# Optimization experiments

Hardware: AMD Instinct MI355X
Metric: run time of the kernel (lower is better)

Reference implementation:

```python
import jax, jax.numpy as jnp
import numpy as np
import math

B, N, DIM = 4, 2048, 512
HEADS, DIM_HEAD = 8, 64
INNER = HEADS * DIM_HEAD  # 512


def setup_inputs() -> dict:
    key = jax.random.key(0)
    ks = jax.random.split(key, 4)
    x = jax.random.normal(ks[0], (B, N, DIM), dtype=jnp.float32)
    # nn.Linear(dim, inner*4, bias=False): store as [dim, 4*inner] for x @ W
    w_qkvg = jax.random.normal(ks[1], (DIM, 4 * INNER), dtype=jnp.float32) * (1.0 / math.sqrt(DIM))
    sigma = jnp.full((1, HEADS, 1, 1), 1.92, dtype=jnp.float32)
    w_out = jax.random.normal(ks[2], (2 * INNER, DIM), dtype=jnp.float32) * (1.0 / math.sqrt(2 * INNER))
    b_out = jax.random.normal(ks[3], (DIM,), dtype=jnp.float32) * 0.01
    return {"x": x, "w_qkvg": w_qkvg, "sigma": sigma, "w_out": w_out, "b_out": b_out}


def reference(x, w_qkvg, sigma, w_out, b_out):
    b, n, d = x.shape
    h, dh = HEADS, DIM_HEAD
    scale = dh ** (-0.5)

    qkvg = x @ w_qkvg  # [b, n, 4*inner]
    q, k, vg, vsigma = jnp.split(qkvg, 4, axis=-1)

    def to_heads(t):  # [b, n, h*dh] -> [b, h, n, dh]
        return t.reshape(b, n, h, dh).transpose(0, 2, 1, 3)

    q, k, vg, vsigma = map(to_heads, (q, k, vg, vsigma))

    # --- softmax branch ---
    dots = jnp.einsum('bhid,bhjd->bhij', q, k) * scale  # [b, h, n, n]
    corr_g = jax.nn.softmax(dots, axis=-1)
    out_g = jnp.matmul(corr_g, vg)  # [b, h, n, dh]

    # --- Gaussian positional-mask branch ---
    pos = jnp.arange(1, n + 1, dtype=x.dtype)
    diffs = jnp.abs(pos[:, None] - pos[None, :])  # [n, n]
    inv_norm = 1.0 / (jnp.sqrt(jnp.asarray(2.0 * math.pi, x.dtype)) * sigma)  # [1, h, 1, 1]
    gm = inv_norm * jnp.exp(-(diffs ** 2)[None, None] / (2.0 * sigma ** 2))  # [1, h, n, n]
    corr_sigma = gm / gm.sum(-1, keepdims=True)
    out_s = jnp.matmul(corr_sigma, vsigma)  # broadcasts over batch -> [b, h, n, dh]

    out = jnp.concatenate([out_g, out_s], axis=-1)  # [b, h, n, 2*dh]
    out = out.transpose(0, 2, 1, 3).reshape(b, n, 2 * h * dh)
    return out @ w_out + b_out
```

## Files before the change

kernel.cpp:

```cpp
#include <hip/hip_runtime.h>

typedef _Float16 f16;
typedef __attribute__((ext_vector_type(8))) _Float16 f16x8;
typedef __attribute__((ext_vector_type(4))) _Float16 f16x4;
typedef __attribute__((ext_vector_type(4))) float f32x4;

#define B_ 4
#define N_ 2048
#define DIM_ 512
#define H_ 8
#define DH_ 64

__device__ __forceinline__ void gload16(const void* g, void* l) {
    __builtin_amdgcn_global_load_lds((const __attribute__((address_space(1))) void*)g,
                                     (__attribute__((address_space(3))) void*)l, 16, 0, 0);
}


__global__ __launch_bounds__(256) void cvt_f16_k8(const float* __restrict__ in,
                                                  f16* __restrict__ out, int n8) {
    int i = blockIdx.x * 256 + threadIdx.x;
    if (i < n8) {
        const float4 a = ((const float4*)in)[i * 2];
        const float4 b = ((const float4*)in)[i * 2 + 1];
        f16x8 o = {(f16)a.x, (f16)a.y, (f16)a.z, (f16)a.w,
                   (f16)b.x, (f16)b.y, (f16)b.z, (f16)b.w};
        ((f16x8*)out)[i] = o;
    }
}

__global__ __launch_bounds__(256) void transpose_cvt_k(const float* __restrict__ in,
                                                       f16* __restrict__ out, int K, int N) {
    __shared__ f16 tile[64][72];
    const int nbk = K >> 6;
    const int bk = blockIdx.x % nbk, bn = blockIdx.x / nbk;
    const int k0 = bk << 6, n0 = bn << 6;
    const int t = threadIdx.x;
    const int r = t >> 2, q = (t & 3) << 4;
#pragma unroll
    for (int u = 0; u < 4; u++) {
        const float4 v = *(const float4*)&in[(size_t)(k0 + r) * N + n0 + q + u * 4];
        tile[q + u * 4 + 0][r] = (f16)v.x;
        tile[q + u * 4 + 1][r] = (f16)v.y;
        tile[q + u * 4 + 2][r] = (f16)v.z;
        tile[q + u * 4 + 3][r] = (f16)v.w;
    }
    __syncthreads();
#pragma unroll
    for (int u = 0; u < 2; u++) {
        f16x8 o = *(const f16x8*)&tile[r][q + u * 8];
        *(f16x8*)&out[(size_t)(n0 + r) * K + k0 + q + u * 8] = o;
    }
}

__global__ __launch_bounds__(512, 2) void gemm0_8ph(
    const f16* __restrict__ A, const f16* __restrict__ BT,
    f16* __restrict__ qb, f16* __restrict__ kb, f16* __restrict__ vbT,
    f16* __restrict__ vs16)
{
    __shared__ char lds[131072];
    const int tid = threadIdx.x;
    const int bid = blockIdx.x;
    const int xcd = bid & 7, w = bid >> 3;
    const int m0 = ((xcd << 2) + (w >> 3)) << 8;
    const int n0 = (w & 7) << 8;
    const int wave = tid >> 6, lane = tid & 63;
    const int wr = wave >> 2, wc = wave & 3;
    const int lr = lane & 15, lg = lane >> 4;

    f32x4 acc[8][4];
    const f32x4 zero = {0.f, 0.f, 0.f, 0.f};
#pragma unroll
    for (int i = 0; i < 8; i++)
#pragma unroll
        for (int j = 0; j < 4; j++) acc[i][j] = zero;

    const f16* gA[2][2]; const f16* gB[2][2];
#pragma unroll
    for (int u = 0; u < 2; u++) {
        int c = tid + u * 512;
        int row = c >> 3;
        int e0 = (((c & 7) ^ (row & 7)) << 3);
#pragma unroll
        for (int h = 0; h < 2; h++) {
            gA[h][u] = A + (size_t)(m0 + h * 128 + row) * 512 + e0;
            gB[h][u] = BT + (size_t)(n0 + h * 128 + row) * 512 + e0;
        }
    }
    const int ldst = wave * 1024;

#pragma unroll
    for (int h = 0; h < 2; h++)
#pragma unroll
        for (int u = 0; u < 2; u++)
            gload16(gA[h][u], lds + h * 16384 + ldst + u * 8192);
#pragma unroll
    for (int h = 0; h < 2; h++)
#pragma unroll
        for (int u = 0; u < 2; u++)
            gload16(gB[h][u], lds + 65536 + h * 16384 + ldst + u * 8192);

    const int swz = (lr & 7) << 4;
    for (int T = 0; T < 8; T++) {
        const int d = T & 1, d2 = (T + 1) & 1;
        const size_t Tn64 = (size_t)(T + 1) * 64;
        const char* Ab = lds + (d * 2 + wr) * 16384;
        const char* Bb = lds + 65536 + (d * 2 + (wc >> 1)) * 16384;
#pragma unroll
        for (int p = 0; p < 4; p++) {
            const int kh = p >> 1, qr = p & 1;
            if (p < 2) {
#pragma unroll
                for (int u = 0; u < 2; u++)
                    gload16(gA[p][u] + Tn64, lds + (d2 * 2 + p) * 16384 + ldst + u * 8192);
            } else {
#pragma unroll
                for (int u = 0; u < 2; u++)
                    gload16(gB[p - 2][u] + Tn64, lds + 65536 + (d2 * 2 + (p - 2)) * 16384 + ldst + u * 8192);
            }
            if (p == 0) {
                asm volatile("s_waitcnt vmcnt(2)" ::: "memory");
            }
            __builtin_amdgcn_s_barrier();

            f16x8 af[4], bf[4];
            const int ko = (kh * 64 + lg * 16) ^ swz;
#pragma unroll
            for (int i = 0; i < 4; i++)
                af[i] = *(const f16x8*)(Ab + (qr * 64 + i * 16 + lr) * 128 + ko);
#pragma unroll
            for (int j = 0; j < 4; j++)
                bf[j] = *(const f16x8*)(Bb + ((wc & 1) * 64 + j * 16 + lr) * 128 + ko);
            asm volatile("s_waitcnt lgkmcnt(0)" ::: "memory");
            __builtin_amdgcn_sched_barrier(0);
            __builtin_amdgcn_s_setprio(1);
#pragma unroll
            for (int i = 0; i < 4; i++)
#pragma unroll
                for (int j = 0; j < 4; j++)
                    acc[qr * 4 + i][j] = __builtin_amdgcn_mfma_f32_16x16x32_f16(af[i], bf[j], acc[qr * 4 + i][j], 0, 0, 0);
            __builtin_amdgcn_s_setprio(0);
            __builtin_amdgcn_s_barrier();
        }
    }

#pragma unroll
    for (int fr = 0; fr < 8; fr++) {
#pragma unroll
        for (int j = 0; j < 4; j++) {
            int col = n0 + wc * 64 + j * 16 + lr;
            int row0 = m0 + wr * 128 + fr * 16 + lg * 4;
            int sec = col >> 9, cc = col & 511;
            int h = cc >> 6, dd = cc & 63;
            int b = row0 >> 11, ns = row0 & 2047;
            if (sec == 2) {
                f16x4 o;
#pragma unroll
                for (int r = 0; r < 4; r++) o[r] = (f16)acc[fr][j][r];
                *(f16x4*)&vbT[((size_t)(b * H_ + h) * DH_ + dd) * N_ + ns] = o;
            } else if (sec == 0) {
#pragma unroll
                for (int r = 0; r < 4; r++)
                    qb[((size_t)(b * H_ + h) * N_ + ns + r) * DH_ + dd] = (f16)(acc[fr][j][r] * 0.1803368801f);
            } else if (sec == 1) {
#pragma unroll
                for (int r = 0; r < 4; r++)
                    kb[((size_t)(b * H_ + h) * N_ + ns + r) * DH_ + dd] = (f16)acc[fr][j][r];
            } else {
#pragma unroll
                for (int r = 0; r < 4; r++)
                    vs16[((size_t)(b * H_ + h) * N_ + ns + r) * DH_ + dd] = (f16)acc[fr][j][r];
            }
        }
    }
}

__global__ __launch_bounds__(256) void gemm_small(
    const f16* __restrict__ A, const f16* __restrict__ BT, int K, int N,
    const float* __restrict__ bias, float* __restrict__ outp)
{
    __shared__ char sAb[8192];
    __shared__ char sBb[8192];
    const int tid = threadIdx.x;
    const int bid = blockIdx.x;
    const int xcd = bid & 7, w = bid >> 3;
    const int m0 = ((xcd << 4) + (w >> 3)) << 6;
    const int n0 = (w & 7) << 6;
    const int wave = tid >> 6, lane = tid & 63;
    const int wr = wave >> 1, wc = wave & 1;
    const int lr = lane & 15, lg = lane >> 4;

    f32x4 acc[2][2];
    const f32x4 zero = {0.f, 0.f, 0.f, 0.f};
#pragma unroll
    for (int i = 0; i < 2; i++)
#pragma unroll
        for (int j = 0; j < 2; j++) acc[i][j] = zero;

    const f16* srcA[2]; const f16* srcB[2];
    char* ldsA[2]; char* ldsB[2];
#pragma unroll
    for (int u = 0; u < 2; u++) {
        int row = wave * 8 + u * 32 + (lane >> 3);
        int e0 = ((lane & 7) ^ (row & 7)) << 3;
        srcA[u] = A + (size_t)(m0 + row) * K + e0;
        srcB[u] = BT + (size_t)(n0 + row) * K + e0;
        ldsA[u] = sAb + wave * 1024 + u * 4096;
        ldsB[u] = sBb + wave * 1024 + u * 4096;
    }

    const int swz = (lr & 7) << 4;
    for (int kt = 0; kt < K; kt += 64) {
#pragma unroll
        for (int u = 0; u < 2; u++) {
            gload16(srcA[u], ldsA[u]);
            gload16(srcB[u], ldsB[u]);
            srcA[u] += 64; srcB[u] += 64;
        }
        __syncthreads();
#pragma unroll
        for (int half = 0; half < 2; half++) {
            f16x8 af[2], bf[2];
#pragma unroll
            for (int i = 0; i < 2; i++) {
                int R = wr * 32 + i * 16 + lr;
                af[i] = *(const f16x8*)(sAb + R * 128 + (((half << 6) | (lg << 4)) ^ swz));
            }
#pragma unroll
            for (int j = 0; j < 2; j++) {
                int R = wc * 32 + j * 16 + lr;
                bf[j] = *(const f16x8*)(sBb + R * 128 + (((half << 6) | (lg << 4)) ^ swz));
            }
#pragma unroll
            for (int i = 0; i < 2; i++)
#pragma unroll
                for (int j = 0; j < 2; j++)
                    acc[i][j] = __builtin_amdgcn_mfma_f32_16x16x32_f16(af[i], bf[j], acc[i][j], 0, 0, 0);
        }
        __syncthreads();
    }

#pragma unroll
    for (int i = 0; i < 2; i++)
#pragma unroll
        for (int j = 0; j < 2; j++) {
            int col = n0 + wc * 32 + j * 16 + lr;
            int row0 = m0 + wr * 32 + i * 16 + lg * 4;
#pragma unroll
            for (int r = 0; r < 4; r++)
                outp[(size_t)(row0 + r) * N + col] = acc[i][j][r] + bias[col];
        }
}

__global__ __launch_bounds__(256) void attn_k(
    const f16* __restrict__ qb, const f16* __restrict__ kb, const f16* __restrict__ vbT,
    f16* __restrict__ cat, f16* __restrict__ oaccB, float* __restrict__ lacc)
{
    __shared__ char sKbf[2 * 8192];
    __shared__ char sVbf[2 * 8192];
    const int tid = threadIdx.x;
    const int bid0 = blockIdx.x;
    const int obid = (bid0 & 7) * 128 + (bid0 >> 3);
    const int bh = obid >> 5, qblk = (obid >> 1) & 15, half = obid & 1;
    const int b = bh >> 3, h = bh & 7;
    const int hn = half << 4;
    const int wave = tid >> 6, lane = tid & 63;
    const int lr = lane & 15, lg = lane >> 4;

    const size_t base = (size_t)bh * N_ * DH_;
    const int qrow_a = qblk * 128 + wave * 32 + lr;
    const int qrow_b = qrow_a + 16;
    const f16x8 qfa0 = *(const f16x8*)&qb[base + (size_t)qrow_a * DH_ + lg * 8];
    const f16x8 qfa1 = *(const f16x8*)&qb[base + (size_t)qrow_a * DH_ + 32 + lg * 8];
    const f16x8 qfb0 = *(const f16x8*)&qb[base + (size_t)qrow_b * DH_ + lg * 8];
    const f16x8 qfb1 = *(const f16x8*)&qb[base + (size_t)qrow_b * DH_ + 32 + lg * 8];

    const f16* kq[2]; const f16* vq[2];
#pragma unroll
    for (int u = 0; u < 2; u++) {
        int row = wave * 8 + u * 32 + (lane >> 3);
        int e0 = ((lane & 7) ^ (row & 7)) << 3;
        kq[u] = kb + base + (size_t)row * 64 + e0;
        vq[u] = vbT + base + (size_t)row * 2048 + e0;
    }
    char* const ldsKw = sKbf + wave * 1024;
    char* const ldsVw = sVbf + wave * 1024;

    f32x4 Ota[4], Otb[4], lacc_a, lacc_b;
    const f32x4 zero = {0.f, 0.f, 0.f, 0.f};
#pragma unroll
    for (int dt = 0; dt < 4; dt++) { Ota[dt] = zero; Otb[dt] = zero; }
    lacc_a = zero; lacc_b = zero;
    const f16x8 ones8 = {(f16)1.f, (f16)1.f, (f16)1.f, (f16)1.f,
                         (f16)1.f, (f16)1.f, (f16)1.f, (f16)1.f};

    const int swz = (lr & 7) << 4;

#pragma unroll
    for (int u = 0; u < 2; u++) gload16(kq[u] + (size_t)hn * 4096, ldsKw + u * 4096);
#pragma unroll
    for (int u = 0; u < 2; u++) gload16(vq[u] + hn * 64, ldsVw + u * 4096);
    asm volatile("s_waitcnt vmcnt(0)" ::: "memory");
    __builtin_amdgcn_s_barrier();

    for (int t = 0; t < 16; t++) {
        {
            const int tn = hn + ((t + 1) & 15);
            char* vdst = ldsVw + ((t + 1) & 1) * 8192;
            char* kdst = ldsKw + ((t + 1) & 1) * 8192;
#pragma unroll
            for (int u = 0; u < 2; u++) gload16(vq[u] + tn * 64, vdst + u * 4096);
#pragma unroll
            for (int u = 0; u < 2; u++) gload16(kq[u] + (size_t)tn * 4096, kdst + u * 4096);
        }

        const char* Kb = sKbf + (t & 1) * 8192;
        const char* Vb = sVbf + (t & 1) * 8192;

        f32x4 sta[4], stb[4];
        __builtin_amdgcn_s_setprio(1);
#pragma unroll
        for (int ct = 0; ct < 4; ct++) {
            int row = ct * 16 + lr;
            f16x8 kf0 = *(const f16x8*)(Kb + (((row << 7) | (lg << 4)) ^ swz));
            f16x8 kf1 = *(const f16x8*)(Kb + (((row << 7) | 64 | (lg << 4)) ^ swz));
            f32x4 sa = __builtin_amdgcn_mfma_f32_16x16x32_f16(kf0, qfa0, zero, 0, 0, 0);
            sta[ct]  = __builtin_amdgcn_mfma_f32_16x16x32_f16(kf1, qfa1, sa, 0, 0, 0);
            f32x4 sb = __builtin_amdgcn_mfma_f32_16x16x32_f16(kf0, qfb0, zero, 0, 0, 0);
            stb[ct]  = __builtin_amdgcn_mfma_f32_16x16x32_f16(kf1, qfb1, sb, 0, 0, 0);
        }
        __builtin_amdgcn_s_setprio(0);

        f16x4 ppa[4], ppb[4];
#pragma unroll
        for (int ct = 0; ct < 4; ct++)
#pragma unroll
            for (int r = 0; r < 4; r++) {
                ppa[ct][r] = (f16)__builtin_amdgcn_exp2f(sta[ct][r]);
                ppb[ct][r] = (f16)__builtin_amdgcn_exp2f(stb[ct][r]);
            }

        __builtin_amdgcn_s_setprio(1);
#pragma unroll
        for (int c = 0; c < 2; c++) {
            f16x8 bfa = __builtin_shufflevector(ppa[2 * c], ppa[2 * c + 1], 0, 1, 2, 3, 4, 5, 6, 7);
            f16x8 bfb = __builtin_shufflevector(ppb[2 * c], ppb[2 * c + 1], 0, 1, 2, 3, 4, 5, 6, 7);
            lacc_a = __builtin_amdgcn_mfma_f32_16x16x32_f16(ones8, bfa, lacc_a, 0, 0, 0);
            lacc_b = __builtin_amdgcn_mfma_f32_16x16x32_f16(ones8, bfb, lacc_b, 0, 0, 0);
#pragma unroll
            for (int dt = 0; dt < 4; dt++) {
                int row = dt * 16 + lr;
                f16x4 vlo = *(const f16x4*)(Vb + (((row << 7) | (c << 6) | (lg << 3)) ^ swz));
                f16x4 vhi = *(const f16x4*)(Vb + (((row << 7) | (c << 6) | 32 | (lg << 3)) ^ swz));
                f16x8 vf = __builtin_shufflevector(vlo, vhi, 0, 1, 2, 3, 4, 5, 6, 7);
                Ota[dt] = __builtin_amdgcn_mfma_f32_16x16x32_f16(vf, bfa, Ota[dt], 0, 0, 0);
                Otb[dt] = __builtin_amdgcn_mfma_f32_16x16x32_f16(vf, bfb, Otb[dt], 0, 0, 0);
            }
        }
        __builtin_amdgcn_s_setprio(0);

        asm volatile("s_waitcnt vmcnt(0)" ::: "memory");
        __builtin_amdgcn_s_barrier();
    }

#pragma unroll
    for (int dt = 0; dt < 4; dt++) {
        f16x4 oa, ob;
#pragma unroll
        for (int r = 0; r < 4; r++) {
            oa[r] = (f16)Ota[dt][r];
            ob[r] = (f16)Otb[dt][r];
        }
        if (half == 0) {
            *(f16x4*)&cat[((size_t)(b * N_ + qrow_a)) * 1024 + h * 128 + dt * 16 + lg * 4] = oa;
            *(f16x4*)&cat[((size_t)(b * N_ + qrow_b)) * 1024 + h * 128 + dt * 16 + lg * 4] = ob;
        } else {
            *(f16x4*)&oaccB[((size_t)(bh * N_ + qrow_a)) * 64 + dt * 16 + lg * 4] = oa;
            *(f16x4*)&oaccB[((size_t)(bh * N_ + qrow_b)) * 64 + dt * 16 + lg * 4] = ob;
        }
    }
    if (lg == 0) {
        lacc[half * (32 * N_) + bh * N_ + qrow_a] = lacc_a[0];
        lacc[half * (32 * N_) + bh * N_ + qrow_b] = lacc_b[0];
    }
}

__global__ __launch_bounds__(256) void combine_k(
    f16* __restrict__ cat, const f16* __restrict__ oaccB, const float* __restrict__ lacc)
{
    int gi = blockIdx.x * 256 + threadIdx.x;
    int row = gi >> 3, c8 = gi & 7;
    int bh = row >> 11, q = row & 2047;
    int b = bh >> 3, h = bh & 7;
    float inv = 1.0f / (lacc[row] + lacc[32 * N_ + row]);
    f16* cp = &cat[((size_t)(b * N_ + q)) * 1024 + h * 128 + c8 * 8];
    f16x8 a = *(const f16x8*)cp;
    f16x8 o2 = *(const f16x8*)&oaccB[(size_t)row * 64 + c8 * 8];
    f16x8 o;
#pragma unroll
    for (int i = 0; i < 8; i++) o[i] = (f16)(((float)a[i] + (float)o2[i]) * inv);
    *(f16x8*)cp = o;
}

__global__ __launch_bounds__(256) void gauss_k(
    const f16* __restrict__ vs16, const float* __restrict__ sigma, f16* __restrict__ cat)
{
    const int tid = threadIdx.x;
    const int bh = blockIdx.y, b = bh >> 3, h = bh & 7;
    const int i0 = blockIdx.x * 64;
    const int wv = tid >> 6, d = tid & 63;
    const float sig = sigma[h];
    const float c = 0.72134752f / (sig * sig);

    float wt[17];
#pragma unroll
    for (int o = 0; o <= 16; o++) wt[o] = __builtin_amdgcn_exp2f(-(float)(o * o) * c);
    float wfull = wt[0];
#pragma unroll
    for (int o = 1; o <= 16; o++) wfull += 2.f * wt[o];
    const float inv_wfull = 1.0f / wfull;

    const size_t base = (size_t)bh * N_ * DH_;
    const int r0 = i0 + wv * 16 - 16;
    float v[48];
#pragma unroll
    for (int k = 0; k < 48; k++) {
        int r = r0 + k; r = r < 0 ? 0 : (r > N_ - 1 ? N_ - 1 : r);
        v[k] = (float)vs16[base + (size_t)r * DH_ + d];
    }

#pragma unroll
    for (int it = 0; it < 16; it++) {
        int i = i0 + wv * 16 + it;
        float acc = 0.f;
        if (i >= 16 && i <= N_ - 17) {
#pragma unroll
            for (int o = -16; o <= 16; o++)
                acc += wt[o < 0 ? -o : o] * v[16 + it + o];
            acc *= inv_wfull;
        } else {
            float ws = 0.f;
#pragma unroll
            for (int o = -16; o <= 16; o++) {
                int j = i + o;
                if (j >= 0 && j <= N_ - 1) {
                    float w = wt[o < 0 ? -o : o];
                    ws += w;
                    acc += w * v[16 + it + o];
                }
            }
            acc /= ws;
        }
        cat[((size_t)(b * N_ + i)) * 1024 + h * 128 + 64 + d] = (f16)acc;
    }
}


extern "C" void kernel_launch(void* const* d_in, const int* in_sizes, int n_in,
                              void* d_out, int out_size, void* d_ws, size_t ws_size,
                              hipStream_t stream) {
    const float* x      = (const float*)d_in[0];
    const float* w_qkvg = (const float*)d_in[1];
    const float* sigma  = (const float*)d_in[2];
    const float* w_out  = (const float*)d_in[3];
    const float* b_out  = (const float*)d_in[4];
    float* out = (float*)d_out;
    char* ws = (char*)d_ws;

    const size_t MB = 1048576;
    f16*   x16  = (f16*)(ws);
    float* lacc = (float*)(ws);
    f16*   wqT  = (f16*)(ws + 8 * MB);
    f16*   woT  = (f16*)(ws + 10 * MB);
    f16*   qb   = (f16*)(ws + 11 * MB);
    f16*   kb   = (f16*)(ws + 19 * MB);
    f16*   vbT  = (f16*)(ws + 27 * MB);
    f16*   vs16 = (f16*)(ws + 35 * MB);
    f16*   cat  = (f16*)(ws + 43 * MB);
    f16*   oaccB= (f16*)(ws + 59 * MB);
    if (ws_size < 67 * MB) return;

    cvt_f16_k8<<<2048, 256, 0, stream>>>(x, x16, B_ * N_ * DIM_ / 8);
    transpose_cvt_k<<<256, 256, 0, stream>>>(w_qkvg, wqT, 512, 2048);
    transpose_cvt_k<<<128, 256, 0, stream>>>(w_out, woT, 1024, 512);

    gemm0_8ph<<<256, 512, 0, stream>>>(x16, wqT, qb, kb, vbT, vs16);

    attn_k<<<1024, 256, 0, stream>>>(qb, kb, vbT, cat, oaccB, lacc);
    combine_k<<<2048, 256, 0, stream>>>(cat, oaccB, lacc);
    gauss_k<<<dim3(32, 32), 256, 0, stream>>>(vs16, sigma, cat);

    gemm_small<<<1024, 256, 0, stream>>>(cat, woT, 1024, 512, b_out, out);
}
```

Before: 120.8 us.

## Load K/V fragments directly from global memory instead of LDS double-buffering

Drops the shared-memory double-buffered staging of K and V tiles (global_load_lds plus barriers) from the attention kernel. Each wave now reads its K and V MFMA fragments straight from global memory through the cache, and the setprio calls are moved to wrap individual MFMA groups. This removes the LDS traffic and per-tile block barriers, but every wave now fetches the same K/V data separately and global-load latency is exposed with no explicit prefetch.

```diff
diff --git a/kernel.cpp b/kernel.cpp
--- a/kernel.cpp
+++ b/kernel.cpp
@@ -256,8 +256,6 @@
     const f16* __restrict__ qb, const f16* __restrict__ kb, const f16* __restrict__ vbT,
     f16* __restrict__ cat, f16* __restrict__ oaccB, float* __restrict__ lacc)
 {
-    __shared__ char sKbf[2 * 8192];
-    __shared__ char sVbf[2 * 8192];
     const int tid = threadIdx.x;
     const int bid0 = blockIdx.x;
     const int obid = (bid0 & 7) * 128 + (bid0 >> 3);
@@ -275,16 +273,8 @@
     const f16x8 qfb0 = *(const f16x8*)&qb[base + (size_t)qrow_b * DH_ + lg * 8];
     const f16x8 qfb1 = *(const f16x8*)&qb[base + (size_t)qrow_b * DH_ + 32 + lg * 8];
 
-    const f16* kq[2]; const f16* vq[2];
-#pragma unroll
-    for (int u = 0; u < 2; u++) {
-        int row = wave * 8 + u * 32 + (lane >> 3);
-        int e0 = ((lane & 7) ^ (row & 7)) << 3;
-        kq[u] = kb + base + (size_t)row * 64 + e0;
-        vq[u] = vbT + base + (size_t)row * 2048 + e0;
-    }
-    char* const ldsKw = sKbf + wave * 1024;
-    char* const ldsVw = sVbf + wave * 1024;
+    const f16* const Kb = kb + base;
+    const f16* const Vb = vbT + base;
 
     f32x4 Ota[4], Otb[4], lacc_a, lacc_b;
     const f32x4 zero = {0.f, 0.f, 0.f, 0.f};
@@ -294,42 +284,26 @@
     const f16x8 ones8 = {(f16)1.f, (f16)1.f, (f16)1.f, (f16)1.f,
                          (f16)1.f, (f16)1.f, (f16)1.f, (f16)1.f};
 
-    const int swz = (lr & 7) << 4;
-
-#pragma unroll
-    for (int u = 0; u < 2; u++) gload16(kq[u] + (size_t)hn * 4096, ldsKw + u * 4096);
-#pragma unroll
-    for (int u = 0; u < 2; u++) gload16(vq[u] + hn * 64, ldsVw + u * 4096);
-    asm volatile("s_waitcnt vmcnt(0)" ::: "memory");
-    __builtin_amdgcn_s_barrier();
+    const f16* vrow[4];
+#pragma unroll
+    for (int dt = 0; dt < 4; dt++) vrow[dt] = Vb + (size_t)(dt * 16 + lr) * N_;
 
     for (int t = 0; t < 16; t++) {
-        {
-            const int tn = hn + ((t + 1) & 15);
-            char* vdst = ldsVw + ((t + 1) & 1) * 8192;
-            char* kdst = ldsKw + ((t + 1) & 1) * 8192;
-#pragma unroll
-            for (int u = 0; u < 2; u++) gload16(vq[u] + tn * 64, vdst + u * 4096);
-#pragma unroll
-            for (int u = 0; u < 2; u++) gload16(kq[u] + (size_t)tn * 4096, kdst + u * 4096);
-        }
-
-        const char* Kb = sKbf + (t & 1) * 8192;
-        const char* Vb = sVbf + (t & 1) * 8192;
+        const int kv0 = (hn + t) << 6;
 
         f32x4 sta[4], stb[4];
-        __builtin_amdgcn_s_setprio(1);
 #pragma unroll
         for (int ct = 0; ct < 4; ct++) {
-            int row = ct * 16 + lr;
-            f16x8 kf0 = *(const f16x8*)(Kb + (((row << 7) | (lg << 4)) ^ swz));
-            f16x8 kf1 = *(const f16x8*)(Kb + (((row << 7) | 64 | (lg << 4)) ^ swz));
+            const f16* kr = Kb + (size_t)(kv0 + ct * 16 + lr) * DH_;
+            f16x8 kf0 = *(const f16x8*)(kr + lg * 8);
+            f16x8 kf1 = *(const f16x8*)(kr + 32 + lg * 8);
+            __builtin_amdgcn_s_setprio(1);
             f32x4 sa = __builtin_amdgcn_mfma_f32_16x16x32_f16(kf0, qfa0, zero, 0, 0, 0);
             sta[ct]  = __builtin_amdgcn_mfma_f32_16x16x32_f16(kf1, qfa1, sa, 0, 0, 0);
             f32x4 sb = __builtin_amdgcn_mfma_f32_16x16x32_f16(kf0, qfb0, zero, 0, 0, 0);
             stb[ct]  = __builtin_amdgcn_mfma_f32_16x16x32_f16(kf1, qfb1, sb, 0, 0, 0);
-        }
-        __builtin_amdgcn_s_setprio(0);
+            __builtin_amdgcn_s_setprio(0);
+        }
 
         f16x4 ppa[4], ppb[4];
 #pragma unroll
@@ -340,27 +314,26 @@
                 ppb[ct][r] = (f16)__builtin_amdgcn_exp2f(stb[ct][r]);
             }
 
-        __builtin_amdgcn_s_setprio(1);
 #pragma unroll
         for (int c = 0; c < 2; c++) {
             f16x8 bfa = __builtin_shufflevector(ppa[2 * c], ppa[2 * c + 1], 0, 1, 2, 3, 4, 5, 6, 7);
             f16x8 bfb = __builtin_shufflevector(ppb[2 * c], ppb[2 * c + 1], 0, 1, 2, 3, 4, 5, 6, 7);
+            __builtin_amdgcn_s_setprio(1);
             lacc_a = __builtin_amdgcn_mfma_f32_16x16x32_f16(ones8, bfa, lacc_a, 0, 0, 0);
             lacc_b = __builtin_amdgcn_mfma_f32_16x16x32_f16(ones8, bfb, lacc_b, 0, 0, 0);
+            __builtin_amdgcn_s_setprio(0);
 #pragma unroll
             for (int dt = 0; dt < 4; dt++) {
-                int row = dt * 16 + lr;
-                f16x4 vlo = *(const f16x4*)(Vb + (((row << 7) | (c << 6) | (lg << 3)) ^ swz));
-                f16x4 vhi = *(const f16x4*)(Vb + (((row << 7) | (c << 6) | 32 | (lg << 3)) ^ swz));
+                const f16* vr = vrow[dt] + kv0 + c * 32 + lg * 4;
+                f16x4 vlo = *(const f16x4*)(vr);
+                f16x4 vhi = *(const f16x4*)(vr + 16);
                 f16x8 vf = __builtin_shufflevector(vlo, vhi, 0, 1, 2, 3, 4, 5, 6, 7);
+                __builtin_amdgcn_s_setprio(1);
                 Ota[dt] = __builtin_amdgcn_mfma_f32_16x16x32_f16(vf, bfa, Ota[dt], 0, 0, 0);
                 Otb[dt] = __builtin_amdgcn_mfma_f32_16x16x32_f16(vf, bfb, Otb[dt], 0, 0, 0);
-            }
-        }
-        __builtin_amdgcn_s_setprio(0);
-
-        asm volatile("s_waitcnt vmcnt(0)" ::: "memory");
-        __builtin_amdgcn_s_barrier();
+                __builtin_amdgcn_s_setprio(0);
+            }
+        }
     }
 
 #pragma unroll
```

Result: slower. 246.1 us (+103.7%).
